# Optimization experiments

Measured on AMD Instinct MI355X. Metric: run time of the kernel, lower is better.

## Reference

```python
import jax, jax.numpy as jnp
import numpy as np

B, N, D = 32, 2048, 1024


def setup_inputs() -> dict:
    key0 = jax.random.key(0)
    ks = jax.random.split(key0, 9)
    scale = 1.0 / np.sqrt(D)
    query = jax.random.normal(ks[0], (B, D), dtype=jnp.float32)
    key = jax.random.normal(ks[1], (B, N, D), dtype=jnp.float32)
    mask = jax.random.randint(ks[2], (B, N), 0, 2, dtype=jnp.int32)
    W1 = jax.random.uniform(ks[3], (D, D), jnp.float32, -scale, scale)
    b1 = jax.random.uniform(ks[4], (D,), jnp.float32, -scale, scale)
    W2 = jax.random.uniform(ks[5], (D, D), jnp.float32, -scale, scale)
    b2 = jax.random.uniform(ks[6], (D,), jnp.float32, -scale, scale)
    v_w = jax.random.uniform(ks[7], (D,), jnp.float32, -scale, scale)
    v_b = jax.random.uniform(ks[8], (), jnp.float32, -scale, scale)
    return {"query": query, "key": key, "mask": mask,
            "W1": W1, "b1": b1, "W2": W2, "b2": b2, "v_w": v_w, "v_b": v_b}


def reference(query, key, mask, W1, b1, W2, b2, v_w, v_b):
    # key_out: [B, N, D] = key @ W1^T + b1 (nn.Linear convention)
    key_out = jnp.einsum('bnd,ed->bne', key, W1) + b1
    # query_out: [B, D] -> broadcast over N
    query_out = jnp.einsum('bd,ed->be', query, W2) + b2
    h = jnp.tanh(key_out + query_out[:, None, :])  # [B, N, D]
    ui = jnp.einsum('bnd,d->bn', h, v_w) + v_b      # v: D -> 1, squeezed
    ui = jnp.where(mask.astype(bool), ui, -jnp.inf)
    return ui
```

## Files before the change

kernel.cpp:

```cpp
#include <hip/hip_runtime.h>
#include <hip/hip_bf16.h>
#include <math.h>

#define B_ 32
#define N_ 2048
#define D_ 1024
#define M_ (B_ * N_)

typedef float  fx4  __attribute__((ext_vector_type(4)));
typedef __bf16 bf16x8 __attribute__((ext_vector_type(8)));
typedef unsigned short us4 __attribute__((ext_vector_type(4)));

#define WS_W1B   134217728ULL
#define WS_T     136314880ULL
#define WS_ACC   136445952ULL

#define MASK_NEG_SENTINEL (-1.0e30f)

__device__ inline unsigned short f2b(float f) {
    __hip_bfloat16 h = __float2bfloat16(f);
    return *reinterpret_cast<unsigned short*>(&h);
}

__global__ void key_convert_kernel(const fx4* __restrict__ key4,
                                   us4* __restrict__ keyb4) {
    const int total = 16777216;
    int idx    = blockIdx.x * blockDim.x + threadIdx.x;
    int stride = gridDim.x * blockDim.x;
    for (int i = idx; i < total; i += stride) {
        fx4 v = key4[i];
        us4 o; o.x = f2b(v.x); o.y = f2b(v.y); o.z = f2b(v.z); o.w = f2b(v.w);
        keyb4[i] = o;
    }
}

__global__ void w1_convert_kernel(const fx4* __restrict__ W1,
                                  us4* __restrict__ w1b4) {
    int idx = blockIdx.x * blockDim.x + threadIdx.x;
#pragma unroll
    for (int i = 0; i < 4; ++i) {
        int j = idx + i * 65536;
        fx4 v = W1[j];
        us4 o; o.x = f2b(v.x); o.y = f2b(v.y); o.z = f2b(v.z); o.w = f2b(v.w);
        w1b4[j] = o;
    }
}

__global__ void tq_kernel(const float* __restrict__ query,
                          const float* __restrict__ W2,
                          const float* __restrict__ b1,
                          const float* __restrict__ b2,
                          float* __restrict__ t) {
    int tid = threadIdx.x;
    int p = blockIdx.x * 32 + (tid >> 3);
    int j = tid & 7;
    int b = p >> 10;
    int e = p & 1023;
    const fx4* q = (const fx4*)query + (size_t)b * 256;
    const fx4* w = (const fx4*)W2 + (size_t)e * 256;
    float acc = 0.f;
#pragma unroll 4
    for (int it = 0; it < 32; ++it) {
        int k4 = it * 8 + j;
        fx4 qv = q[k4];
        fx4 wv = w[k4];
        acc += qv.x * wv.x + qv.y * wv.y + qv.z * wv.z + qv.w * wv.w;
    }
    acc += __shfl_xor(acc, 1);
    acc += __shfl_xor(acc, 2);
    acc += __shfl_xor(acc, 4);
    if (j == 0) t[p] = acc + b1[e] + b2[e];
}

__device__ inline float fast_tanh(float x) {
    float ax = fabsf(x);
    float e  = __expf(-2.0f * ax);
    float r  = (1.0f - e) / (1.0f + e);
    return copysignf(r, x);
}

#define BM 128
#define BN 128
#define BK 32

#define GLD16(g, l)                                                        \
    __builtin_amdgcn_global_load_lds(                                      \
        (const __attribute__((address_space(1))) void*)(g),                \
        (__attribute__((address_space(3))) void*)(l), 16, 0, 0)

__global__ void __launch_bounds__(256)
main_gemm(const unsigned short* __restrict__ keyb,
          const unsigned short* __restrict__ w1b,
          const float* __restrict__ t,
          const float* __restrict__ v_w,
          float* __restrict__ accum) {
    __shared__ unsigned short As[BM * BK];
    __shared__ unsigned short Bs[BN * BK];

    const int tid  = threadIdx.x;
    const int lane = tid & 63;
    const int wave = tid >> 6;
    const int quad = lane >> 4;
    const int l15  = lane & 15;
    const int m0 = blockIdx.y * BM;
    const int e0 = blockIdx.x * BN;
    const int mw = (wave >> 1) * 64;
    const int ew = (wave & 1) * 64;

    const int srow  = tid >> 2;
    const int skoff = (tid & 3) * 8;
    const unsigned short* aSrc0 = keyb + (size_t)(m0 + srow) * D_ + skoff;
    const unsigned short* aSrc1 = aSrc0 + (size_t)64 * D_;
    const unsigned short* bSrc0 = w1b + (size_t)(e0 + srow) * D_ + skoff;
    const unsigned short* bSrc1 = bSrc0 + (size_t)64 * D_;
    char* AsB = (char*)As;
    char* BsB = (char*)Bs;
    char* aDst0 = AsB + wave * 1024;
    char* aDst1 = AsB + 4096 + wave * 1024;
    char* bDst0 = BsB + wave * 1024;
    char* bDst1 = BsB + 4096 + wave * 1024;

    fx4 acc[4][4] = {};

    for (int k0 = 0; k0 < D_; k0 += BK) {
        GLD16(aSrc0 + k0, aDst0);
        GLD16(aSrc1 + k0, aDst1);
        GLD16(bSrc0 + k0, bDst0);
        GLD16(bSrc1 + k0, bDst1);
        __syncthreads();

        bf16x8 a[4], b[4];
#pragma unroll
        for (int i = 0; i < 4; ++i) {
            int ml = mw + i * 16 + l15;
            a[i] = *(const bf16x8*)(&As[ml * BK + quad * 8]);
        }
#pragma unroll
        for (int j = 0; j < 4; ++j) {
            int el = ew + j * 16 + l15;
            b[j] = *(const bf16x8*)(&Bs[el * BK + quad * 8]);
        }
#pragma unroll
        for (int i = 0; i < 4; ++i)
#pragma unroll
            for (int j = 0; j < 4; ++j)
                acc[i][j] = __builtin_amdgcn_mfma_f32_16x16x32_bf16(
                    a[i], b[j], acc[i][j], 0, 0, 0);

        __syncthreads();
    }

    const float* trow = t + (size_t)(m0 >> 11) * D_;
    float vwv[4], tqv[4];
#pragma unroll
    for (int j = 0; j < 4; ++j) {
        int e = e0 + ew + j * 16 + l15;
        vwv[j] = v_w[e];
        tqv[j] = trow[e];
    }
#pragma unroll
    for (int i = 0; i < 4; ++i) {
#pragma unroll
        for (int r = 0; r < 4; ++r) {
            float s = 0.f;
#pragma unroll
            for (int j = 0; j < 4; ++j)
                s += vwv[j] * fast_tanh(acc[i][j][r] + tqv[j]);
            s += __shfl_xor(s, 1);
            s += __shfl_xor(s, 2);
            s += __shfl_xor(s, 4);
            s += __shfl_xor(s, 8);
            if (l15 == 0) {
                int m = m0 + mw + i * 16 + quad * 4 + r;
                atomicAdd(&accum[m], s);
            }
        }
    }
}

__global__ void finalize_kernel(const float* __restrict__ accum,
                                const int* __restrict__ mask,
                                const float* __restrict__ v_b,
                                float* __restrict__ out) {
    int i = blockIdx.x * blockDim.x + threadIdx.x;
    if (i < M_) {
        float vb = v_b[0];
        out[i] = mask[i] ? (accum[i] + vb) : MASK_NEG_SENTINEL;
    }
}

extern "C" void kernel_launch(void* const* d_in, const int* in_sizes, int n_in,
                              void* d_out, int out_size, void* d_ws, size_t ws_size,
                              hipStream_t stream) {
    const float* query = (const float*)d_in[0];
    const float* key   = (const float*)d_in[1];
    const int*   mask  = (const int*)d_in[2];
    const float* W1    = (const float*)d_in[3];
    const float* b1    = (const float*)d_in[4];
    const float* W2    = (const float*)d_in[5];
    const float* b2    = (const float*)d_in[6];
    const float* v_w   = (const float*)d_in[7];
    const float* v_b   = (const float*)d_in[8];

    char* ws = (char*)d_ws;
    unsigned short* keyb = (unsigned short*)ws;
    unsigned short* w1b  = (unsigned short*)(ws + WS_W1B);
    float*          t    = (float*)(ws + WS_T);
    float*          acc  = (float*)(ws + WS_ACC);

    key_convert_kernel<<<4096, 256, 0, stream>>>((const fx4*)key, (us4*)keyb);
    w1_convert_kernel<<<256, 256, 0, stream>>>((const fx4*)W1, (us4*)w1b);
    tq_kernel<<<1024, 256, 0, stream>>>(query, W2, b1, b2, t);
    hipMemsetAsync(acc, 0, (size_t)M_ * sizeof(float), stream);
    dim3 g(8, 512);
    main_gemm<<<g, 256, 0, stream>>>(keyb, w1b, t, v_w, acc);
    finalize_kernel<<<M_ / 256, 256, 0, stream>>>(acc, mask, v_b, (float*)d_out);
}
```

Baseline: 611.3 us.

## Fuse prep kernels and loop all E tiles per block to drop atomics

The key conversion, W1 conversion and query projection kernels are merged into one launch that splits work by block index. The main GEMM now gives each block a 128-row M tile and loops over all eight 128-wide E tiles. It accumulates the tanh/v_w row sums in registers, reduces them through shared memory and writes the masked output directly. This removes the memset, the atomicAdd traffic and the separate finalize kernel. The trade-off is that the GEMM grid shrinks from 4096 to 512 blocks, which lowers parallelism and occupancy for the main matmul.

```diff
diff --git a/kernel.cpp b/kernel.cpp
--- a/kernel.cpp
+++ b/kernel.cpp
@@ -13,7 +13,6 @@
 
 #define WS_W1B   134217728ULL
 #define WS_T     136314880ULL
-#define WS_ACC   136445952ULL
 
 #define MASK_NEG_SENTINEL (-1.0e30f)
 
@@ -22,54 +21,55 @@
     return *reinterpret_cast<unsigned short*>(&h);
 }
 
-__global__ void key_convert_kernel(const fx4* __restrict__ key4,
-                                   us4* __restrict__ keyb4) {
-    const int total = 16777216;
-    int idx    = blockIdx.x * blockDim.x + threadIdx.x;
-    int stride = gridDim.x * blockDim.x;
-    for (int i = idx; i < total; i += stride) {
-        fx4 v = key4[i];
-        us4 o; o.x = f2b(v.x); o.y = f2b(v.y); o.z = f2b(v.z); o.w = f2b(v.w);
-        keyb4[i] = o;
+__global__ void prep_kernel(const fx4* __restrict__ key4,
+                            us4* __restrict__ keyb4,
+                            const fx4* __restrict__ W14,
+                            us4* __restrict__ w1b4,
+                            const float* __restrict__ query,
+                            const float* __restrict__ W2,
+                            const float* __restrict__ b1,
+                            const float* __restrict__ b2,
+                            float* __restrict__ t) {
+    const int bx  = blockIdx.x;
+    const int tid = threadIdx.x;
+    if (bx < 4096) {
+        int base = bx * 256 + tid;
+#pragma unroll
+        for (int c = 0; c < 16; ++c) {
+            int i = base + c * 1048576;
+            fx4 v = key4[i];
+            us4 o; o.x = f2b(v.x); o.y = f2b(v.y); o.z = f2b(v.z); o.w = f2b(v.w);
+            keyb4[i] = o;
+        }
+    } else if (bx < 4352) {
+        int idx = (bx - 4096) * 256 + tid;
+#pragma unroll
+        for (int c = 0; c < 4; ++c) {
+            int j = idx + c * 65536;
+            fx4 v = W14[j];
+            us4 o; o.x = f2b(v.x); o.y = f2b(v.y); o.z = f2b(v.z); o.w = f2b(v.w);
+            w1b4[j] = o;
+        }
+    } else {
+        int p = (bx - 4352) * 32 + (tid >> 3);
+        int j = tid & 7;
+        int b = p >> 10;
+        int e = p & 1023;
+        const fx4* q = (const fx4*)query + (size_t)b * 256;
+        const fx4* w = (const fx4*)W2 + (size_t)e * 256;
+        float acc = 0.f;
+#pragma unroll 4
+        for (int it = 0; it < 32; ++it) {
+            int k4 = it * 8 + j;
+            fx4 qv = q[k4];
+            fx4 wv = w[k4];
+            acc += qv.x * wv.x + qv.y * wv.y + qv.z * wv.z + qv.w * wv.w;
+        }
+        acc += __shfl_xor(acc, 1);
+        acc += __shfl_xor(acc, 2);
+        acc += __shfl_xor(acc, 4);
+        if (j == 0) t[p] = acc + b1[e] + b2[e];
     }
-}
-
-__global__ void w1_convert_kernel(const fx4* __restrict__ W1,
-                                  us4* __restrict__ w1b4) {
-    int idx = blockIdx.x * blockDim.x + threadIdx.x;
-#pragma unroll
-    for (int i = 0; i < 4; ++i) {
-        int j = idx + i * 65536;
-        fx4 v = W1[j];
-        us4 o; o.x = f2b(v.x); o.y = f2b(v.y); o.z = f2b(v.z); o.w = f2b(v.w);
-        w1b4[j] = o;
-    }
-}
-
-__global__ void tq_kernel(const float* __restrict__ query,
-                          const float* __restrict__ W2,
-                          const float* __restrict__ b1,
-                          const float* __restrict__ b2,
-                          float* __restrict__ t) {
-    int tid = threadIdx.x;
-    int p = blockIdx.x * 32 + (tid >> 3);
-    int j = tid & 7;
-    int b = p >> 10;
-    int e = p & 1023;
-    const fx4* q = (const fx4*)query + (size_t)b * 256;
-    const fx4* w = (const fx4*)W2 + (size_t)e * 256;
-    float acc = 0.f;
-#pragma unroll 4
-    for (int it = 0; it < 32; ++it) {
-        int k4 = it * 8 + j;
-        fx4 qv = q[k4];
-        fx4 wv = w[k4];
-        acc += qv.x * wv.x + qv.y * wv.y + qv.z * wv.z + qv.w * wv.w;
-    }
-    acc += __shfl_xor(acc, 1);
-    acc += __shfl_xor(acc, 2);
-    acc += __shfl_xor(acc, 4);
-    if (j == 0) t[p] = acc + b1[e] + b2[e];
 }
 
 __device__ inline float fast_tanh(float x) {
@@ -82,6 +82,7 @@
 #define BM 128
 #define BN 128
 #define BK 32
+#define NET 8
 
 #define GLD16(g, l)                                                        \
     __builtin_amdgcn_global_load_lds(                                      \
@@ -93,17 +94,19 @@
           const unsigned short* __restrict__ w1b,
           const float* __restrict__ t,
           const float* __restrict__ v_w,
-          float* __restrict__ accum) {
+          const int* __restrict__ mask,
+          const float* __restrict__ v_b,
+          float* __restrict__ out) {
     __shared__ unsigned short As[BM * BK];
     __shared__ unsigned short Bs[BN * BK];
+    __shared__ float rowsum[2][BM];
 
     const int tid  = threadIdx.x;
     const int lane = tid & 63;
     const int wave = tid >> 6;
     const int quad = lane >> 4;
     const int l15  = lane & 15;
-    const int m0 = blockIdx.y * BM;
-    const int e0 = blockIdx.x * BN;
+    const int m0 = blockIdx.x * BM;
     const int mw = (wave >> 1) * 64;
     const int ew = (wave & 1) * 64;
 
@@ -111,8 +114,8 @@
     const int skoff = (tid & 3) * 8;
     const unsigned short* aSrc0 = keyb + (size_t)(m0 + srow) * D_ + skoff;
     const unsigned short* aSrc1 = aSrc0 + (size_t)64 * D_;
-    const unsigned short* bSrc0 = w1b + (size_t)(e0 + srow) * D_ + skoff;
-    const unsigned short* bSrc1 = bSrc0 + (size_t)64 * D_;
+    const unsigned short* bSrcB = w1b + (size_t)srow * D_ + skoff;
+
     char* AsB = (char*)As;
     char* BsB = (char*)Bs;
     char* aDst0 = AsB + wave * 1024;
@@ -120,72 +123,80 @@
     char* bDst0 = BsB + wave * 1024;
     char* bDst1 = BsB + 4096 + wave * 1024;
 
-    fx4 acc[4][4] = {};
-
-    for (int k0 = 0; k0 < D_; k0 += BK) {
-        GLD16(aSrc0 + k0, aDst0);
-        GLD16(aSrc1 + k0, aDst1);
-        GLD16(bSrc0 + k0, bDst0);
-        GLD16(bSrc1 + k0, bDst1);
-        __syncthreads();
-
-        bf16x8 a[4], b[4];
-#pragma unroll
-        for (int i = 0; i < 4; ++i) {
-            int ml = mw + i * 16 + l15;
-            a[i] = *(const bf16x8*)(&As[ml * BK + quad * 8]);
-        }
+    const float* trow = t + (size_t)(m0 >> 11) * D_;
+
+    float srowacc[4][4];
+#pragma unroll
+    for (int i = 0; i < 4; ++i)
+#pragma unroll
+        for (int r = 0; r < 4; ++r) srowacc[i][r] = 0.f;
+
+    for (int et = 0; et < NET; ++et) {
+        const unsigned short* bSrc0 = bSrcB + (size_t)et * 128 * D_;
+        const unsigned short* bSrc1 = bSrc0 + (size_t)64 * D_;
+
+        fx4 acc[4][4] = {};
+
+        for (int k0 = 0; k0 < D_; k0 += BK) {
+            GLD16(aSrc0 + k0, aDst0);
+            GLD16(aSrc1 + k0, aDst1);
+            GLD16(bSrc0 + k0, bDst0);
+            GLD16(bSrc1 + k0, bDst1);
+            __syncthreads();
+
+            bf16x8 a[4], b[4];
+#pragma unroll
+            for (int i = 0; i < 4; ++i)
+                a[i] = *(const bf16x8*)(&As[(mw + i * 16 + l15) * BK + quad * 8]);
+#pragma unroll
+            for (int j = 0; j < 4; ++j)
+                b[j] = *(const bf16x8*)(&Bs[(ew + j * 16 + l15) * BK + quad * 8]);
+#pragma unroll
+            for (int i = 0; i < 4; ++i)
+#pragma unroll
+                for (int j = 0; j < 4; ++j)
+                    acc[i][j] = __builtin_amdgcn_mfma_f32_16x16x32_bf16(
+                        a[i], b[j], acc[i][j], 0, 0, 0);
+
+            __syncthreads();
+        }
+
+        float vwv[4], tqv[4];
 #pragma unroll
         for (int j = 0; j < 4; ++j) {
-            int el = ew + j * 16 + l15;
-            b[j] = *(const bf16x8*)(&Bs[el * BK + quad * 8]);
+            int e = et * 128 + ew + j * 16 + l15;
+            vwv[j] = v_w[e];
+            tqv[j] = trow[e];
         }
 #pragma unroll
         for (int i = 0; i < 4; ++i)
 #pragma unroll
-            for (int j = 0; j < 4; ++j)
-                acc[i][j] = __builtin_amdgcn_mfma_f32_16x16x32_bf16(
-                    a[i], b[j], acc[i][j], 0, 0, 0);
-
-        __syncthreads();
+            for (int r = 0; r < 4; ++r) {
+                float s = 0.f;
+#pragma unroll
+                for (int j = 0; j < 4; ++j)
+                    s += vwv[j] * fast_tanh(acc[i][j][r] + tqv[j]);
+                srowacc[i][r] += s;
+            }
     }
 
-    const float* trow = t + (size_t)(m0 >> 11) * D_;
-    float vwv[4], tqv[4];
-#pragma unroll
-    for (int j = 0; j < 4; ++j) {
-        int e = e0 + ew + j * 16 + l15;
-        vwv[j] = v_w[e];
-        tqv[j] = trow[e];
-    }
-#pragma unroll
-    for (int i = 0; i < 4; ++i) {
+#pragma unroll
+    for (int i = 0; i < 4; ++i)
 #pragma unroll
         for (int r = 0; r < 4; ++r) {
-            float s = 0.f;
-#pragma unroll
-            for (int j = 0; j < 4; ++j)
-                s += vwv[j] * fast_tanh(acc[i][j][r] + tqv[j]);
+            float s = srowacc[i][r];
             s += __shfl_xor(s, 1);
             s += __shfl_xor(s, 2);
             s += __shfl_xor(s, 4);
             s += __shfl_xor(s, 8);
-            if (l15 == 0) {
-                int m = m0 + mw + i * 16 + quad * 4 + r;
-                atomicAdd(&accum[m], s);
-            }
-        }
-    }
-}
-
-__global__ void finalize_kernel(const float* __restrict__ accum,
-                                const int* __restrict__ mask,
-                                const float* __restrict__ v_b,
-                                float* __restrict__ out) {
-    int i = blockIdx.x * blockDim.x + threadIdx.x;
-    if (i < M_) {
-        float vb = v_b[0];
-        out[i] = mask[i] ? (accum[i] + vb) : MASK_NEG_SENTINEL;
+            if (l15 == 0)
+                rowsum[wave & 1][mw + i * 16 + quad * 4 + r] = s;
+        }
+    __syncthreads();
+    if (tid < BM) {
+        int m = m0 + tid;
+        float v = rowsum[0][tid] + rowsum[1][tid] + v_b[0];
+        out[m] = mask[m] ? v : MASK_NEG_SENTINEL;
     }
 }
 
@@ -206,13 +217,10 @@
     unsigned short* keyb = (unsigned short*)ws;
     unsigned short* w1b  = (unsigned short*)(ws + WS_W1B);
     float*          t    = (float*)(ws + WS_T);
-    float*          acc  = (float*)(ws + WS_ACC);
-
-    key_convert_kernel<<<4096, 256, 0, stream>>>((const fx4*)key, (us4*)keyb);
-    w1_convert_kernel<<<256, 256, 0, stream>>>((const fx4*)W1, (us4*)w1b);
-    tq_kernel<<<1024, 256, 0, stream>>>(query, W2, b1, b2, t);
-    hipMemsetAsync(acc, 0, (size_t)M_ * sizeof(float), stream);
-    dim3 g(8, 512);
-    main_gemm<<<g, 256, 0, stream>>>(keyb, w1b, t, v_w, acc);
-    finalize_kernel<<<M_ / 256, 256, 0, stream>>>(acc, mask, v_b, (float*)d_out);
-}
+
+    prep_kernel<<<5376, 256, 0, stream>>>((const fx4*)key, (us4*)keyb,
+                                          (const fx4*)W1, (us4*)w1b,
+                                          query, W2, b1, b2, t);
+    main_gemm<<<512, 256, 0, stream>>>(keyb, w1b, t, v_w, mask, v_b,
+                                       (float*)d_out);
+}
```

After: 802.4 us. 1.31x slower.
